# Kernel tuning notes

Hardware: AMD Instinct MI355X
Metric: run time of the kernel (lower is better)

## Reference

```python
import jax, jax.numpy as jnp
import numpy as np
import math

B, S, D, H, L = 256, 256, 256, 4, 2
DH = D // H
NITEMS = 50000
EPS = 1e-5


def setup_inputs() -> dict:
    key = jax.random.key(0)
    ks = jax.random.split(key, 16)
    w = lambda k, shape, scale: (jax.random.normal(k, shape, jnp.float32) * scale)
    return {
        "input_ids": jax.random.randint(ks[0], (B, S), 0, NITEMS),
        "item_emb": w(ks[1], (NITEMS, D), 0.02),
        "pos_emb": w(ks[2], (S, D), 0.02),
        "Wq": w(ks[3], (L, D, D), 0.05),
        "bq": jnp.zeros((L, D), jnp.float32),
        "Wk": w(ks[4], (L, D, D), 0.05),
        "bk": jnp.zeros((L, D), jnp.float32),
        "Wv": w(ks[5], (L, D, D), 0.05),
        "bv": jnp.zeros((L, D), jnp.float32),
        "Wo": w(ks[6], (L, D, D), 0.05),
        "bo": jnp.zeros((L, D), jnp.float32),
        "W1": w(ks[7], (L, D, 4 * D), 0.05),
        "b1": jnp.zeros((L, 4 * D), jnp.float32),
        "W2": w(ks[8], (L, 4 * D, D), 0.05),
        "b2": jnp.zeros((L, D), jnp.float32),
    }


def _layer_norm(x):
    mu = jnp.mean(x, axis=-1, keepdims=True)
    var = jnp.mean(jnp.square(x - mu), axis=-1, keepdims=True)
    return (x - mu) * jax.lax.rsqrt(var + EPS)


def reference(input_ids, item_emb, pos_emb, Wq, bq, Wk, bk, Wv, bv,
              Wo, bo, W1, b1, W2, b2):
    Bn, Sn = input_ids.shape
    dtype = item_emb.dtype
    # attention bias: padding (id>0) AND causal; (1-mask)*-10000
    pad = (input_ids > 0).astype(dtype)                       # [B,S]
    causal = jnp.tril(jnp.ones((Sn, Sn), dtype))              # [S,S]
    mask = pad[:, None, None, :] * causal[None, None]         # [B,1,S,S]
    attn_bias = (1.0 - mask) * -10000.0

    # input embedding (dropout is identity in eval)
    x = _layer_norm(item_emb[input_ids] + pos_emb[None])      # [B,S,D]
    total = x
    scale = 1.0 / math.sqrt(DH)

    for l in range(L):
        # --- self-attention ---
        def heads(z):  # [B,S,D] -> [B,H,S,DH]
            return z.reshape(Bn, Sn, H, DH).transpose(0, 2, 1, 3)
        q = heads(x @ Wq[l] + bq[l])
        k = heads(x @ Wk[l] + bk[l])
        v = heads(x @ Wv[l] + bv[l])
        scores = jnp.einsum('bhqd,bhkd->bhqk', q, k) * scale + attn_bias
        probs = jax.nn.softmax(scores, axis=-1)
        ctx = jnp.einsum('bhqk,bhkd->bhqd', probs, v)
        ctx = ctx.transpose(0, 2, 1, 3).reshape(Bn, Sn, D)
        h = _layer_norm(ctx @ Wo[l] + bo[l] + x)
        # --- FFN (no residual in IntermediateLayer) ---
        ffn = jax.nn.gelu(h @ W1[l] + b1[l], approximate=False) @ W2[l] + b2[l]
        x = _layer_norm(ffn)
        total = total + x

    return total
```

## Files before the change

### kernel.cpp

```cpp
#include <hip/hip_runtime.h>
#include <math.h>

typedef __attribute__((ext_vector_type(8))) short short8;
typedef __attribute__((ext_vector_type(4))) short shortx4;
typedef __attribute__((ext_vector_type(4))) int   intx4;
typedef __attribute__((ext_vector_type(4))) float floatx4;

#define BQ 256
#define SQ 256
#define DQ 256
#define HQ 4
#define DHQ 64

__device__ __forceinline__ short f2bf(float f) {
  union { float f; unsigned u; } c; c.f = f;
  unsigned r = c.u + 0x7fffu + ((c.u >> 16) & 1u);
  return (short)(r >> 16);
}
__device__ __forceinline__ float bf2f(short s) {
  union { unsigned u; float f; } c; c.u = ((unsigned)(unsigned short)s) << 16;
  return c.f;
}
__device__ __forceinline__ float gelu_fast(float x) {
  float t = x * (0.7978845608f + 0.0356774081f * x * x);
  return x / (1.0f + __expf(-2.0f * t));
}

__global__ __launch_bounds__(256) void wconv_kernel(const float* __restrict__ W,
    short* __restrict__ Wt, int K, int N, int total) {
  int idx = blockIdx.x * 256 + threadIdx.x;
  if (idx >= total) return;
  int nk = N * K;
  int l = idx / nk;
  int r = idx - l * nk;
  int n = r / K;
  int k = r - n * K;
  Wt[idx] = f2bf(W[(size_t)l * nk + (size_t)k * N + n]);
}

__global__ __launch_bounds__(256) void bconv_kernel(const float* __restrict__ bq,
    const float* __restrict__ bk, const float* __restrict__ bv, float* __restrict__ dst) {
  int i = blockIdx.x * 256 + threadIdx.x;
  int l = i / 768, r = i - l * 768;
  const float* src = (r < 256) ? bq : ((r < 512) ? bk : bv);
  dst[i] = src[l * 256 + (r & 255)];
}

__global__ __launch_bounds__(256) void embed_kernel(const int* __restrict__ ids,
    const float* __restrict__ item, const float* __restrict__ pos,
    short* __restrict__ xb, float* __restrict__ tot) {
  const int tid = threadIdx.x, lane = tid & 63, w = tid >> 6;
  const int row = blockIdx.x * 4 + w;
  const int s = row & (SQ - 1);
  const int id = ids[row];
  floatx4 a = *(const floatx4*)(item + (size_t)id * DQ + lane * 4);
  floatx4 p = *(const floatx4*)(pos + (size_t)s * DQ + lane * 4);
  float v[4];
#pragma unroll
  for (int i = 0; i < 4; ++i) v[i] = a[i] + p[i];
  float sm = v[0] + v[1] + v[2] + v[3];
  float ss = v[0]*v[0] + v[1]*v[1] + v[2]*v[2] + v[3]*v[3];
#pragma unroll
  for (int off = 32; off; off >>= 1) { sm += __shfl_xor(sm, off); ss += __shfl_xor(ss, off); }
  float mu = sm * (1.0f / DQ);
  float var = ss * (1.0f / DQ) - mu * mu;
  float rs = rsqrtf(var + 1e-5f);
  shortx4 o; floatx4 y;
#pragma unroll
  for (int i = 0; i < 4; ++i) { y[i] = (v[i] - mu) * rs; o[i] = f2bf(y[i]); }
  *(shortx4*)(xb + (size_t)row * DQ + lane * 4) = o;
  *(floatx4*)(tot + (size_t)row * DQ + lane * 4) = y;
}

__device__ __forceinline__ void async16(const void* g, void* l) {
  __builtin_amdgcn_global_load_lds(
      (const __attribute__((address_space(1))) void*)g,
      (__attribute__((address_space(3))) void*)l, 16, 0, 0);
}

__global__ __launch_bounds__(512, 4) void gemm_kernel(
    const short* __restrict__ A, const short* __restrict__ Bt,
    const float* __restrict__ bias, const short* __restrict__ res,
    short* __restrict__ out, float* __restrict__ tot,
    int M, int N, int K, int act, int ln, int chunked) {
  __shared__ short smem[12288];
  short* As = smem;
  short* Bs = smem + 4096;
  float* redS  = (float*)(smem + 8448);
  float* redS2 = redS + 512;
  const int tid = threadIdx.x, lane = tid & 63, w = tid >> 6;
  const int lane15 = lane & 15, quad = lane >> 4;
  const int wm = w & 1, wn = w >> 1;
  const int bm = blockIdx.y, bn = blockIdx.x;

  const short* Ag = A + (size_t)(bm * 128 + w * 16 + (lane >> 2)) * K + (lane & 3) * 8;
  const short* Bg0 = Bt + (size_t)(bn * 256 + w * 32 + (lane >> 2)) * K + (lane & 3) * 8;
  const short* Bg1 = Bg0 + (size_t)16 * K;

  floatx4 acc[4][4] = {};
  const int nk = K >> 5;
  for (int kb = 0; kb < nk; ++kb) {
    const int k0 = kb * 32;
    async16(Ag + k0, &As[w * 512]);
    async16(Bg0 + k0, &Bs[w * 1024]);
    async16(Bg1 + k0, &Bs[w * 1024 + 512]);
    __syncthreads();
    short8 af[4], bfr[4];
#pragma unroll
    for (int i = 0; i < 4; ++i) {
      af[i]  = *(const short8*)&As[(wm * 64 + i * 16 + lane15) * 32 + quad * 8];
      bfr[i] = *(const short8*)&Bs[(wn * 64 + i * 16 + lane15) * 32 + quad * 8];
    }
#pragma unroll
    for (int i = 0; i < 4; ++i)
#pragma unroll
      for (int j = 0; j < 4; ++j)
        acc[i][j] = __builtin_amdgcn_mfma_f32_16x16x32_bf16(bfr[j], af[i], acc[i][j], 0, 0, 0);
    __syncthreads();
  }

  float sum_[4], sq_[4];
#pragma unroll
  for (int i = 0; i < 4; ++i) { sum_[i] = 0.0f; sq_[i] = 0.0f; }
#pragma unroll
  for (int i = 0; i < 4; ++i) {
    size_t rowg = (size_t)bm * 128 + wm * 64 + i * 16 + lane15;
#pragma unroll
    for (int j = 0; j < 4; ++j) {
      int nloc = wn * 64 + j * 16 + quad * 4;
      floatx4 b4 = *(const floatx4*)(bias + bn * 256 + nloc);
      shortx4 r4;
      if (res) r4 = *(const shortx4*)(res + rowg * 256 + nloc);
#pragma unroll
      for (int r = 0; r < 4; ++r) {
        float z = acc[i][j][r] + b4[r];
        if (res) z += bf2f(r4[r]);
        if (act) z = gelu_fast(z);
        acc[i][j][r] = z;
        if (ln) { sum_[i] += z; sq_[i] += z * z; }
      }
    }
  }

  if (ln) {
#pragma unroll
    for (int i = 0; i < 4; ++i) {
      sum_[i] += __shfl_xor(sum_[i], 16); sum_[i] += __shfl_xor(sum_[i], 32);
      sq_[i]  += __shfl_xor(sq_[i], 16);  sq_[i]  += __shfl_xor(sq_[i], 32);
    }
    if (quad == 0) {
#pragma unroll
      for (int i = 0; i < 4; ++i) {
        int lr = wm * 64 + i * 16 + lane15;
        redS[lr * 4 + wn] = sum_[i];
        redS2[lr * 4 + wn] = sq_[i];
      }
    }
    __syncthreads();
#pragma unroll
    for (int i = 0; i < 4; ++i) {
      int lr = wm * 64 + i * 16 + lane15;
      float s = redS[lr * 4] + redS[lr * 4 + 1] + redS[lr * 4 + 2] + redS[lr * 4 + 3];
      float q = redS2[lr * 4] + redS2[lr * 4 + 1] + redS2[lr * 4 + 2] + redS2[lr * 4 + 3];
      float mu = s * (1.0f / 256.0f);
      float var = q * (1.0f / 256.0f) - mu * mu;
      float rs = rsqrtf(var + 1e-5f);
      size_t rowg = (size_t)bm * 128 + wm * 64 + i * 16 + lane15;
#pragma unroll
      for (int j = 0; j < 4; ++j) {
        int nloc = wn * 64 + j * 16 + quad * 4;
        floatx4 y;
#pragma unroll
        for (int r = 0; r < 4; ++r) y[r] = (acc[i][j][r] - mu) * rs;
        acc[i][j] = y;
        if (tot) {
          floatx4* tp = (floatx4*)(tot + rowg * 256 + nloc);
          floatx4 t = *tp;
#pragma unroll
          for (int r = 0; r < 4; ++r) t[r] += y[r];
          *tp = t;
        }
      }
    }
  }

#pragma unroll
  for (int i = 0; i < 4; ++i) {
    __syncthreads();
    int lr = wm * 16 + lane15;
#pragma unroll
    for (int j = 0; j < 4; ++j) {
      shortx4 o;
#pragma unroll
      for (int r = 0; r < 4; ++r) o[r] = f2bf(acc[i][j][r]);
      *(shortx4*)&smem[lr * 264 + wn * 64 + j * 16 + quad * 4] = o;
    }
    __syncthreads();
#pragma unroll
    for (int it = 0; it < 2; ++it) {
      int t2 = tid + it * 512;
      int lr2 = t2 >> 5, c = (t2 & 31) * 8;
      short8 v = *(const short8*)&smem[lr2 * 264 + c];
      size_t rowg = (size_t)bm * 128 + (lr2 >> 4) * 64 + i * 16 + (lr2 & 15);
      short* dst = chunked ? out + (size_t)bn * M * 256 + rowg * 256 + c
                           : out + rowg * (size_t)N + bn * 256 + c;
      *(short8*)dst = v;
    }
  }
}

__global__ __launch_bounds__(256) void attn_kernel(
    const short* __restrict__ qg, const short* __restrict__ kg, const short* __restrict__ vg,
    const int* __restrict__ ids, short* __restrict__ ctxg) {
  __shared__ short lds[32768];
  const int tid = threadIdx.x, lane = tid & 63, w = tid >> 6;
  const int lane15 = lane & 15, quad = lane >> 4;
  const int bx = blockIdx.x;
  const int qt = bx & 3, h = (bx >> 2) & 3, b = bx >> 4;
  const int base_row = b * SQ;
  const int hcol = h * DHQ;

  for (int it = 0; it < 8; ++it) {
    int s = it * 32 + (tid >> 3);
    int d0 = (tid & 7) * 8;
    size_t goff = (size_t)(base_row + s) * DQ + hcol + d0;
    intx4 kv = *(const intx4*)(kg + goff);
    *(intx4*)&lds[(d0 >> 5) * 8192 + s * 32 + (d0 & 31)] = kv;
    short8 vv = *(const short8*)(vg + goff);
    int vb0 = 16384 + (s >> 5) * 2048 + (s & 31);
#pragma unroll
    for (int i = 0; i < 8; ++i) lds[vb0 + (d0 + i) * 32] = vv[i];
  }
  __syncthreads();

  const int q0 = qt * 64 + w * 16;
  short8 qf[2];
#pragma unroll
  for (int ks = 0; ks < 2; ++ks)
    qf[ks] = *(const short8*)(qg + (size_t)(base_row + q0 + lane15) * DQ + hcol + ks * 32 + quad * 8);

  float sc[16][4];
#pragma unroll
  for (int t = 0; t < 16; ++t) {
    floatx4 a = {0.f, 0.f, 0.f, 0.f};
#pragma unroll
    for (int ks = 0; ks < 2; ++ks) {
      short8 bfr = *(const short8*)&lds[ks * 8192 + (t * 16 + lane15) * 32 + quad * 8];
      a = __builtin_amdgcn_mfma_f32_16x16x32_bf16(qf[ks], bfr, a, 0, 0, 0);
    }
    int kk = t * 16 + lane15;
    int padv = ids[base_row + kk];
#pragma unroll
    for (int r = 0; r < 4; ++r) {
      int q = q0 + quad * 4 + r;
      float bias = (padv > 0 && kk <= q) ? 0.0f : -10000.0f;
      sc[t][r] = a[r] * 0.125f + bias;
    }
  }
  __syncthreads();

#pragma unroll
  for (int r = 0; r < 4; ++r) {
    float m = -1e30f;
#pragma unroll
    for (int t = 0; t < 16; ++t) m = fmaxf(m, sc[t][r]);
    m = fmaxf(m, __shfl_xor(m, 1)); m = fmaxf(m, __shfl_xor(m, 2));
    m = fmaxf(m, __shfl_xor(m, 4)); m = fmaxf(m, __shfl_xor(m, 8));
    float l = 0.0f;
#pragma unroll
    for (int t = 0; t < 16; ++t) { sc[t][r] = __expf(sc[t][r] - m); l += sc[t][r]; }
    l += __shfl_xor(l, 1); l += __shfl_xor(l, 2);
    l += __shfl_xor(l, 4); l += __shfl_xor(l, 8);
    float inv = 1.0f / l;
#pragma unroll
    for (int t = 0; t < 16; ++t)
      lds[w * 4096 + (t >> 1) * 512 + (quad * 4 + r) * 32 + (t & 1) * 16 + lane15] =
          f2bf(sc[t][r] * inv);
  }
  __syncthreads();

  floatx4 o[4] = {};
#pragma unroll
  for (int kb = 0; kb < 8; ++kb) {
    short8 pf = *(const short8*)&lds[w * 4096 + kb * 512 + lane15 * 32 + quad * 8];
#pragma unroll
    for (int dt = 0; dt < 4; ++dt) {
      short8 vf = *(const short8*)&lds[16384 + kb * 2048 + (dt * 16 + lane15) * 32 + quad * 8];
      o[dt] = __builtin_amdgcn_mfma_f32_16x16x32_bf16(pf, vf, o[dt], 0, 0, 0);
    }
  }
#pragma unroll
  for (int dt = 0; dt < 4; ++dt)
#pragma unroll
    for (int r = 0; r < 4; ++r) {
      int q = q0 + quad * 4 + r;
      ctxg[(size_t)(base_row + q) * DQ + hcol + dt * 16 + lane15] = f2bf(o[dt][r]);
    }
}

extern "C" void kernel_launch(void* const* d_in, const int* in_sizes, int n_in,
                              void* d_out, int out_size, void* d_ws, size_t ws_size,
                              hipStream_t stream) {
  const int*   ids  = (const int*)d_in[0];
  const float* item = (const float*)d_in[1];
  const float* pos  = (const float*)d_in[2];
  const float* Wq = (const float*)d_in[3];  const float* bq = (const float*)d_in[4];
  const float* Wk = (const float*)d_in[5];  const float* bk = (const float*)d_in[6];
  const float* Wv = (const float*)d_in[7];  const float* bv = (const float*)d_in[8];
  const float* Wo = (const float*)d_in[9];  const float* bo = (const float*)d_in[10];
  const float* W1 = (const float*)d_in[11]; const float* b1 = (const float*)d_in[12];
  const float* W2 = (const float*)d_in[13]; const float* b2 = (const float*)d_in[14];
  float* out = (float*)d_out;

  const size_t EL = (size_t)BQ * SQ * DQ;
  short* qb    = (short*)d_ws;
  short* kb    = qb + EL;
  short* vb    = kb + EL;
  short* ctxb  = vb + EL;
  short* gb    = qb;
  short* xb    = ctxb + EL;
  short* hb    = xb + EL;
  short* WqkvT = hb + EL;
  short* WoT   = WqkvT + 2 * 3 * 65536;
  short* W1T   = WoT + 2 * 65536;
  short* W2T   = W1T + 2 * 262144;
  float* bqkv  = (float*)(W2T + 2 * 262144);

  const int M = BQ * SQ;

  for (int l = 0; l < 2; ++l) {
    wconv_kernel<<<256, 256, 0, stream>>>(Wq + l * 65536, WqkvT + (l * 3 + 0) * 65536, 256, 256, 65536);
    wconv_kernel<<<256, 256, 0, stream>>>(Wk + l * 65536, WqkvT + (l * 3 + 1) * 65536, 256, 256, 65536);
    wconv_kernel<<<256, 256, 0, stream>>>(Wv + l * 65536, WqkvT + (l * 3 + 2) * 65536, 256, 256, 65536);
  }
  wconv_kernel<<<512, 256, 0, stream>>>(Wo, WoT, 256, 256, 131072);
  wconv_kernel<<<2048, 256, 0, stream>>>(W1, W1T, 256, 1024, 524288);
  wconv_kernel<<<2048, 256, 0, stream>>>(W2, W2T, 1024, 256, 524288);
  bconv_kernel<<<6, 256, 0, stream>>>(bq, bk, bv, bqkv);

  embed_kernel<<<M / 4, 256, 0, stream>>>(ids, item, pos, xb, out);

  for (int l = 0; l < 2; ++l) {
    gemm_kernel<<<dim3(3, M / 128), 512, 0, stream>>>(
        xb, WqkvT + (size_t)l * 3 * 65536, bqkv + l * 768, nullptr, qb, nullptr,
        M, 768, 256, 0, 0, 1);
    attn_kernel<<<BQ * HQ * (SQ / 64), 256, 0, stream>>>(qb, kb, vb, ids, ctxb);
    gemm_kernel<<<dim3(1, M / 128), 512, 0, stream>>>(
        ctxb, WoT + (size_t)l * 65536, bo + l * 256, xb, hb, nullptr,
        M, 256, 256, 0, 1, 0);
    gemm_kernel<<<dim3(4, M / 128), 512, 0, stream>>>(
        hb, W1T + (size_t)l * 262144, b1 + l * 1024, nullptr, gb, nullptr,
        M, 1024, 256, 1, 0, 0);
    gemm_kernel<<<dim3(1, M / 128), 512, 0, stream>>>(
        gb, W2T + (size_t)l * 262144, b2 + l * 256, nullptr, xb, out,
        M, 256, 1024, 0, 1, 0);
  }
}
```

Baseline: 815.3 us.

## Rewrite attention as causal flash-style with V-transpose from QKV GEMM and LDS swizzles

Attention becomes an online-softmax loop over 64-key tiles. Each block handles 128 queries and skips key tiles above the causal diagonal, with K and V tiles double-buffered through async global-to-LDS loads. The QKV GEMM now writes V already transposed so attention no longer scatters it element by element into LDS, and the GEMM LDS reads use an XOR swizzle to avoid bank conflicts. The three QKV weight conversions are merged into a single launch. The cost is more complex attention code with online-softmax rescaling, and a transpose epilogue in the GEMM.

```diff
diff --git a/kernel.cpp b/kernel.cpp
--- a/kernel.cpp
+++ b/kernel.cpp
@@ -24,6 +24,12 @@
 __device__ __forceinline__ float gelu_fast(float x) {
   float t = x * (0.7978845608f + 0.0356774081f * x * x);
   return x / (1.0f + __expf(-2.0f * t));
+}
+
+__device__ __forceinline__ void async16(const void* g, void* l) {
+  __builtin_amdgcn_global_load_lds(
+      (const __attribute__((address_space(1))) void*)g,
+      (__attribute__((address_space(3))) void*)l, 16, 0, 0);
 }
 
 __global__ __launch_bounds__(256) void wconv_kernel(const float* __restrict__ W,
@@ -38,6 +44,18 @@
   Wt[idx] = f2bf(W[(size_t)l * nk + (size_t)k * N + n]);
 }
 
+__global__ __launch_bounds__(256) void wconv_qkv_kernel(const float* __restrict__ Wq,
+    const float* __restrict__ Wk, const float* __restrict__ Wv, short* __restrict__ Wt) {
+  int idx = blockIdx.x * 256 + threadIdx.x;
+  int l = idx / 196608;
+  int r = idx - l * 196608;
+  int which = r / 65536;
+  int e = r & 65535;
+  int n = e >> 8, k = e & 255;
+  const float* W = (which == 0) ? Wq : ((which == 1) ? Wk : Wv);
+  Wt[idx] = f2bf(W[l * 65536 + k * 256 + n]);
+}
+
 __global__ __launch_bounds__(256) void bconv_kernel(const float* __restrict__ bq,
     const float* __restrict__ bk, const float* __restrict__ bv, float* __restrict__ dst) {
   int i = blockIdx.x * 256 + threadIdx.x;
@@ -72,16 +90,10 @@
   *(floatx4*)(tot + (size_t)row * DQ + lane * 4) = y;
 }
 
-__device__ __forceinline__ void async16(const void* g, void* l) {
-  __builtin_amdgcn_global_load_lds(
-      (const __attribute__((address_space(1))) void*)g,
-      (__attribute__((address_space(3))) void*)l, 16, 0, 0);
-}
-
 __global__ __launch_bounds__(512, 4) void gemm_kernel(
     const short* __restrict__ A, const short* __restrict__ Bt,
     const float* __restrict__ bias, const short* __restrict__ res,
-    short* __restrict__ out, float* __restrict__ tot,
+    short* __restrict__ out, float* __restrict__ tot, short* __restrict__ vt,
     int M, int N, int K, int act, int ln, int chunked) {
   __shared__ short smem[12288];
   short* As = smem;
@@ -93,9 +105,14 @@
   const int wm = w & 1, wn = w >> 1;
   const int bm = blockIdx.y, bn = blockIdx.x;
 
-  const short* Ag = A + (size_t)(bm * 128 + w * 16 + (lane >> 2)) * K + (lane & 3) * 8;
-  const short* Bg0 = Bt + (size_t)(bn * 256 + w * 32 + (lane >> 2)) * K + (lane & 3) * 8;
+  const int rA = lane >> 2;
+  const int swzA = (rA & 3) ^ ((rA >> 2) & 3);
+  const int gA = ((lane & 3) ^ swzA) * 8;
+  const short* Ag  = A  + (size_t)(bm * 128 + w * 16 + rA) * K + gA;
+  const short* Bg0 = Bt + (size_t)(bn * 256 + w * 32 + rA) * K + gA;
   const short* Bg1 = Bg0 + (size_t)16 * K;
+
+  const int qs = ((quad ^ ((lane15 & 3) ^ ((lane15 >> 2) & 3))) * 8);
 
   floatx4 acc[4][4] = {};
   const int nk = K >> 5;
@@ -108,8 +125,8 @@
     short8 af[4], bfr[4];
 #pragma unroll
     for (int i = 0; i < 4; ++i) {
-      af[i]  = *(const short8*)&As[(wm * 64 + i * 16 + lane15) * 32 + quad * 8];
-      bfr[i] = *(const short8*)&Bs[(wn * 64 + i * 16 + lane15) * 32 + quad * 8];
+      af[i]  = *(const short8*)&As[(wm * 64 + i * 16 + lane15) * 32 + qs];
+      bfr[i] = *(const short8*)&Bs[(wn * 64 + i * 16 + lane15) * 32 + qs];
     }
 #pragma unroll
     for (int i = 0; i < 4; ++i)
@@ -184,6 +201,8 @@
     }
   }
 
+  const int vtrans = (vt != nullptr) && (bn == 2);
+
 #pragma unroll
   for (int i = 0; i < 4; ++i) {
     __syncthreads();
@@ -196,106 +215,176 @@
       *(shortx4*)&smem[lr * 264 + wn * 64 + j * 16 + quad * 4] = o;
     }
     __syncthreads();
-#pragma unroll
-    for (int it = 0; it < 2; ++it) {
-      int t2 = tid + it * 512;
-      int lr2 = t2 >> 5, c = (t2 & 31) * 8;
-      short8 v = *(const short8*)&smem[lr2 * 264 + c];
-      size_t rowg = (size_t)bm * 128 + (lr2 >> 4) * 64 + i * 16 + (lr2 & 15);
-      short* dst = chunked ? out + (size_t)bn * M * 256 + rowg * 256 + c
-                           : out + rowg * (size_t)N + bn * 256 + c;
-      *(short8*)dst = v;
-    }
-  }
-}
-
-__global__ __launch_bounds__(256) void attn_kernel(
-    const short* __restrict__ qg, const short* __restrict__ kg, const short* __restrict__ vg,
-    const int* __restrict__ ids, short* __restrict__ ctxg) {
-  __shared__ short lds[32768];
+    if (vtrans) {
+      int d = tid & 255;
+      int grp = tid >> 8;
+      short vv[16];
+#pragma unroll
+      for (int rr = 0; rr < 16; ++rr) vv[rr] = smem[(grp * 16 + rr) * 264 + d];
+      size_t row = ((size_t)((bm >> 1) * 256 + d)) * 256 + (bm & 1) * 128 + grp * 64 + i * 16;
+      *(short8*)(vt + row) = *(short8*)&vv[0];
+      *(short8*)(vt + row + 8) = *(short8*)&vv[8];
+    } else {
+#pragma unroll
+      for (int it = 0; it < 2; ++it) {
+        int t2 = tid + it * 512;
+        int lr2 = t2 >> 5, c = (t2 & 31) * 8;
+        short8 v = *(const short8*)&smem[lr2 * 264 + c];
+        size_t rowg = (size_t)bm * 128 + (lr2 >> 4) * 64 + i * 16 + (lr2 & 15);
+        short* dst = chunked ? out + (size_t)bn * M * 256 + rowg * 256 + c
+                             : out + rowg * (size_t)N + bn * 256 + c;
+        *(short8*)dst = v;
+      }
+    }
+  }
+}
+
+__global__ __launch_bounds__(256, 4) void attn_kernel(
+    const short* __restrict__ qg, const short* __restrict__ kg,
+    const short* __restrict__ vtg, const int* __restrict__ ids,
+    short* __restrict__ ctxg) {
+  __shared__ short lds[20480];
   const int tid = threadIdx.x, lane = tid & 63, w = tid >> 6;
   const int lane15 = lane & 15, quad = lane >> 4;
+  const int l7 = lane15 & 7;
   const int bx = blockIdx.x;
-  const int qt = bx & 3, h = (bx >> 2) & 3, b = bx >> 4;
-  const int base_row = b * SQ;
-  const int hcol = h * DHQ;
-
-  for (int it = 0; it < 8; ++it) {
-    int s = it * 32 + (tid >> 3);
-    int d0 = (tid & 7) * 8;
-    size_t goff = (size_t)(base_row + s) * DQ + hcol + d0;
-    intx4 kv = *(const intx4*)(kg + goff);
-    *(intx4*)&lds[(d0 >> 5) * 8192 + s * 32 + (d0 & 31)] = kv;
-    short8 vv = *(const short8*)(vg + goff);
-    int vb0 = 16384 + (s >> 5) * 2048 + (s & 31);
-#pragma unroll
-    for (int i = 0; i < 8; ++i) lds[vb0 + (d0 + i) * 32] = vv[i];
-  }
-  __syncthreads();
-
-  const int q0 = qt * 64 + w * 16;
-  short8 qf[2];
-#pragma unroll
-  for (int ks = 0; ks < 2; ++ks)
-    qf[ks] = *(const short8*)(qg + (size_t)(base_row + q0 + lane15) * DQ + hcol + ks * 32 + quad * 8);
-
-  float sc[16][4];
-#pragma unroll
-  for (int t = 0; t < 16; ++t) {
-    floatx4 a = {0.f, 0.f, 0.f, 0.f};
-#pragma unroll
-    for (int ks = 0; ks < 2; ++ks) {
-      short8 bfr = *(const short8*)&lds[ks * 8192 + (t * 16 + lane15) * 32 + quad * 8];
-      a = __builtin_amdgcn_mfma_f32_16x16x32_bf16(qf[ks], bfr, a, 0, 0, 0);
-    }
-    int kk = t * 16 + lane15;
-    int padv = ids[base_row + kk];
+  const int qh = bx & 1, h = (bx >> 1) & 3, b = bx >> 3;
+  const int kbmax = qh * 2 + 1;
+
+  short8 qf[2][2];
+#pragma unroll
+  for (int t = 0; t < 2; ++t) {
+    int q0 = qh * 128 + t * 64 + w * 16;
+#pragma unroll
+    for (int ks = 0; ks < 2; ++ks)
+      qf[t][ks] = *(const short8*)(qg + (size_t)(b * 256 + q0 + lane15) * 256 +
+                                   h * 64 + ks * 32 + quad * 8);
+  }
+
+  float m_[2][4], l_[2][4];
+  floatx4 o[2][4];
+#pragma unroll
+  for (int t = 0; t < 2; ++t)
 #pragma unroll
     for (int r = 0; r < 4; ++r) {
-      int q = q0 + quad * 4 + r;
-      float bias = (padv > 0 && kk <= q) ? 0.0f : -10000.0f;
-      sc[t][r] = a[r] * 0.125f + bias;
-    }
-  }
-  __syncthreads();
-
-#pragma unroll
-  for (int r = 0; r < 4; ++r) {
-    float m = -1e30f;
-#pragma unroll
-    for (int t = 0; t < 16; ++t) m = fmaxf(m, sc[t][r]);
-    m = fmaxf(m, __shfl_xor(m, 1)); m = fmaxf(m, __shfl_xor(m, 2));
-    m = fmaxf(m, __shfl_xor(m, 4)); m = fmaxf(m, __shfl_xor(m, 8));
-    float l = 0.0f;
-#pragma unroll
-    for (int t = 0; t < 16; ++t) { sc[t][r] = __expf(sc[t][r] - m); l += sc[t][r]; }
-    l += __shfl_xor(l, 1); l += __shfl_xor(l, 2);
-    l += __shfl_xor(l, 4); l += __shfl_xor(l, 8);
-    float inv = 1.0f / l;
-#pragma unroll
-    for (int t = 0; t < 16; ++t)
-      lds[w * 4096 + (t >> 1) * 512 + (quad * 4 + r) * 32 + (t & 1) * 16 + lane15] =
-          f2bf(sc[t][r] * inv);
-  }
-  __syncthreads();
-
-  floatx4 o[4] = {};
-#pragma unroll
-  for (int kb = 0; kb < 8; ++kb) {
-    short8 pf = *(const short8*)&lds[w * 4096 + kb * 512 + lane15 * 32 + quad * 8];
-#pragma unroll
-    for (int dt = 0; dt < 4; ++dt) {
-      short8 vf = *(const short8*)&lds[16384 + kb * 2048 + (dt * 16 + lane15) * 32 + quad * 8];
-      o[dt] = __builtin_amdgcn_mfma_f32_16x16x32_bf16(pf, vf, o[dt], 0, 0, 0);
-    }
-  }
-#pragma unroll
-  for (int dt = 0; dt < 4; ++dt)
+      m_[t][r] = -1e30f; l_[t][r] = 0.0f;
+#pragma unroll
+      for (int dt = 0; dt < 4; ++dt) o[t][dt][r] = 0.0f;
+    }
+
+  const int srow = w * 8 + (lane >> 3);
+  const int g8 = ((lane & 7) ^ (srow & 7)) * 8;
+  const short* kgp = kg + (size_t)(b * 256 + srow) * 256 + h * 64 + g8;
+  const short* vgp = vtg + (size_t)(b * 256 + h * 64 + srow) * 256 + g8;
+  short* pbuf = &lds[16384 + w * 1024];
+
+#define STAGE_TILE(kb_, ib_)                                                       \
+  do {                                                                             \
+    async16(kgp + (size_t)(kb_) * 64 * 256,        &lds[(ib_) * 4096 + w * 512]);  \
+    async16(kgp + (size_t)((kb_) * 64 + 32) * 256, &lds[(ib_) * 4096 + 2048 + w * 512]); \
+    async16(vgp + (kb_) * 64,            &lds[8192 + (ib_) * 4096 + w * 512]);     \
+    async16(vgp + 32 * 256 + (kb_) * 64, &lds[8192 + (ib_) * 4096 + 2048 + w * 512]); \
+  } while (0)
+
+  STAGE_TILE(0, 0);
+
+  for (int kb = 0; kb <= kbmax; ++kb) {
+    __syncthreads();
+    if (kb < kbmax) {
+      int ib = (kb + 1) & 1;
+      STAGE_TILE(kb + 1, ib);
+    }
+    const short* kbuf = &lds[(kb & 1) * 4096];
+    const short* vbuf = &lds[8192 + (kb & 1) * 4096];
+
+    float padb[4];
+#pragma unroll
+    for (int t16 = 0; t16 < 4; ++t16)
+      padb[t16] = (ids[b * 256 + kb * 64 + t16 * 16 + lane15] > 0) ? 0.0f : -10000.0f;
+
+#pragma unroll
+    for (int t = 0; t < 2; ++t) {
+      if (qh * 2 + t < kb) continue;
+      const int q0 = qh * 128 + t * 64 + w * 16;
+      const int diag = (qh * 2 + t == kb);
+      floatx4 e[4];
+#pragma unroll
+      for (int t16 = 0; t16 < 4; ++t16) {
+        floatx4 a = {0.f, 0.f, 0.f, 0.f};
+#pragma unroll
+        for (int ks = 0; ks < 2; ++ks) {
+          short8 kf = *(const short8*)&kbuf[(t16 * 16 + lane15) * 64 +
+                                            (((ks * 4 + quad) ^ l7) * 8)];
+          a = __builtin_amdgcn_mfma_f32_16x16x32_bf16(qf[t][ks], kf, a, 0, 0, 0);
+        }
+        if (diag) {
+          int kk = kb * 64 + t16 * 16 + lane15;
+#pragma unroll
+          for (int r = 0; r < 4; ++r) {
+            int q = q0 + quad * 4 + r;
+            e[t16][r] = a[r] * 0.125f + ((kk <= q) ? padb[t16] : -10000.0f);
+          }
+        } else {
+#pragma unroll
+          for (int r = 0; r < 4; ++r) e[t16][r] = a[r] * 0.125f + padb[t16];
+        }
+      }
+#pragma unroll
+      for (int r = 0; r < 4; ++r) {
+        float mx = fmaxf(fmaxf(e[0][r], e[1][r]), fmaxf(e[2][r], e[3][r]));
+        mx = fmaxf(mx, __shfl_xor(mx, 1));
+        mx = fmaxf(mx, __shfl_xor(mx, 2));
+        mx = fmaxf(mx, __shfl_xor(mx, 4));
+        mx = fmaxf(mx, __shfl_xor(mx, 8));
+        float mn = fmaxf(m_[t][r], mx);
+        float alpha = __expf(m_[t][r] - mn);
+        m_[t][r] = mn;
+        float s = 0.0f;
+#pragma unroll
+        for (int t16 = 0; t16 < 4; ++t16) {
+          float ev = __expf(e[t16][r] - mn);
+          e[t16][r] = ev;
+          s += ev;
+        }
+        s += __shfl_xor(s, 1); s += __shfl_xor(s, 2);
+        s += __shfl_xor(s, 4); s += __shfl_xor(s, 8);
+        l_[t][r] = l_[t][r] * alpha + s;
+#pragma unroll
+        for (int dt = 0; dt < 4; ++dt) o[t][dt][r] *= alpha;
+        int qloc = quad * 4 + r;
+        int swq = (qloc & 7) ^ (qloc >> 2);
+#pragma unroll
+        for (int t16 = 0; t16 < 4; ++t16) {
+          int slot = (t16 * 2 + (lane15 >> 3)) ^ swq;
+          pbuf[qloc * 64 + slot * 8 + l7] = f2bf(e[t16][r]);
+        }
+      }
+#pragma unroll
+      for (int kb2 = 0; kb2 < 2; ++kb2) {
+        short8 pf = *(const short8*)&pbuf[lane15 * 64 +
+                      ((((kb2 * 4 + quad) ^ l7 ^ (lane15 >> 2)) * 8))];
+#pragma unroll
+        for (int dt = 0; dt < 4; ++dt) {
+          short8 vf = *(const short8*)&vbuf[(dt * 16 + lane15) * 64 +
+                        (((kb2 * 4 + quad) ^ l7) * 8)];
+          o[t][dt] = __builtin_amdgcn_mfma_f32_16x16x32_bf16(pf, vf, o[t][dt], 0, 0, 0);
+        }
+      }
+    }
+  }
+
+#pragma unroll
+  for (int t = 0; t < 2; ++t) {
+    const int q0 = qh * 128 + t * 64 + w * 16;
 #pragma unroll
     for (int r = 0; r < 4; ++r) {
-      int q = q0 + quad * 4 + r;
-      ctxg[(size_t)(base_row + q) * DQ + hcol + dt * 16 + lane15] = f2bf(o[dt][r]);
-    }
+      float inv = 1.0f / l_[t][r];
+      size_t row = (size_t)(b * 256 + q0 + quad * 4 + r) * 256 + h * 64;
+#pragma unroll
+      for (int dt = 0; dt < 4; ++dt)
+        ctxg[row + dt * 16 + lane15] = f2bf(o[t][dt][r] * inv);
+    }
+  }
 }
 
 extern "C" void kernel_launch(void* const* d_in, const int* in_sizes, int n_in,
@@ -315,8 +404,8 @@
   const size_t EL = (size_t)BQ * SQ * DQ;
   short* qb    = (short*)d_ws;
   short* kb    = qb + EL;
-  short* vb    = kb + EL;
-  short* ctxb  = vb + EL;
+  short* vt    = kb + EL;
+  short* ctxb  = vt + EL;
   short* gb    = qb;
   short* xb    = ctxb + EL;
   short* hb    = xb + EL;
@@ -328,11 +417,7 @@
 
   const int M = BQ * SQ;
 
-  for (int l = 0; l < 2; ++l) {
-    wconv_kernel<<<256, 256, 0, stream>>>(Wq + l * 65536, WqkvT + (l * 3 + 0) * 65536, 256, 256, 65536);
-    wconv_kernel<<<256, 256, 0, stream>>>(Wk + l * 65536, WqkvT + (l * 3 + 1) * 65536, 256, 256, 65536);
-    wconv_kernel<<<256, 256, 0, stream>>>(Wv + l * 65536, WqkvT + (l * 3 + 2) * 65536, 256, 256, 65536);
-  }
+  wconv_qkv_kernel<<<1536, 256, 0, stream>>>(Wq, Wk, Wv, WqkvT);
   wconv_kernel<<<512, 256, 0, stream>>>(Wo, WoT, 256, 256, 131072);
   wconv_kernel<<<2048, 256, 0, stream>>>(W1, W1T, 256, 1024, 524288);
   wconv_kernel<<<2048, 256, 0, stream>>>(W2, W2T, 1024, 256, 524288);
@@ -342,17 +427,17 @@
 
   for (int l = 0; l < 2; ++l) {
     gemm_kernel<<<dim3(3, M / 128), 512, 0, stream>>>(
-        xb, WqkvT + (size_t)l * 3 * 65536, bqkv + l * 768, nullptr, qb, nullptr,
+        xb, WqkvT + (size_t)l * 3 * 65536, bqkv + l * 768, nullptr, qb, nullptr, vt,
         M, 768, 256, 0, 0, 1);
-    attn_kernel<<<BQ * HQ * (SQ / 64), 256, 0, stream>>>(qb, kb, vb, ids, ctxb);
+    attn_kernel<<<BQ * HQ * 2, 256, 0, stream>>>(qb, kb, vt, ids, ctxb);
     gemm_kernel<<<dim3(1, M / 128), 512, 0, stream>>>(
-        ctxb, WoT + (size_t)l * 65536, bo + l * 256, xb, hb, nullptr,
+        ctxb, WoT + (size_t)l * 65536, bo + l * 256, xb, hb, nullptr, nullptr,
         M, 256, 256, 0, 1, 0);
     gemm_kernel<<<dim3(4, M / 128), 512, 0, stream>>>(
-        hb, W1T + (size_t)l * 262144, b1 + l * 1024, nullptr, gb, nullptr,
+        hb, W1T + (size_t)l * 262144, b1 + l * 1024, nullptr, gb, nullptr, nullptr,
         M, 1024, 256, 1, 0, 0);
     gemm_kernel<<<dim3(1, M / 128), 512, 0, stream>>>(
-        gb, W2T + (size_t)l * 262144, b2 + l * 256, nullptr, xb, out,
+        gb, W2T + (size_t)l * 262144, b2 + l * 256, nullptr, xb, out, nullptr,
         M, 256, 1024, 0, 1, 0);
   }
 }
```

After: 867.1 us. 6.4% more time.
